# Kernel tuning notes

Hardware: AMD Instinct MI355X
Metric: run time of the kernel (lower is better)

Reference implementation:

```python
import jax, jax.numpy as jnp
import numpy as np

DILATIONS = (48, 76, 96, 111, 124, 135, 144, 152)


def setup_inputs() -> dict:
    key = jax.random.key(0)
    kx, kw, kb = jax.random.split(key, 3)
    B_, C_IN, H, Wd = 8, 64, 128, 512
    C_OUT = 64
    x = jax.random.normal(kx, (B_, C_IN, H, Wd), dtype=jnp.float32)
    # stacked weights for 8 parallel branches: [branch, out_ch, in_ch, kh=1, kw=3]
    W = jax.random.normal(kw, (8, C_OUT, C_IN, 1, 3), dtype=jnp.float32) * 0.05
    B = jax.random.normal(kb, (8, C_OUT), dtype=jnp.float32) * 0.05
    return {"x": x, "W": W, "B": B}


def _dilated_conv(x, w, d):
    # 'same' padding for kernel (1,3) with dilation (1,d): pad d on each side of width
    return jax.lax.conv_general_dilated(
        x, w,
        window_strides=(1, 1),
        padding=[(0, 0), (d, d)],
        rhs_dilation=(1, d),
        dimension_numbers=("NCHW", "OIHW", "NCHW"),
    )


def reference(x, W, B):
    out = None
    for i, d in enumerate(DILATIONS):  # fixed small structural loop over branches
        y = _dilated_conv(x, W[i], d) + B[i][None, :, None, None]
        out = y if out is None else out + y
    return jax.nn.relu(out)
```

## Files before the change

kernel.cpp:

```cpp
#include <hip/hip_runtime.h>
#include <hip/hip_bf16.h>
#include <stdint.h>

typedef float  f32x4 __attribute__((ext_vector_type(4)));
typedef short  s16x8 __attribute__((ext_vector_type(8)));

#define NB    8
#define CIN   64
#define COUT  64
#define HH    128
#define WW    512
#define NTAP  17
#define PADW  152
#define XROW  816
#define BUFB  (XROW * 64)
#define HW    (HH * WW)

__global__ __launch_bounds__(256) void prep_wfrag(
        const float* __restrict__ W, const float* __restrict__ Bv,
        __hip_bfloat16* __restrict__ wf, float* __restrict__ bsum) {
    int idx = blockIdx.x * 256 + threadIdx.x;
    if (idx < NTAP * 2 * 4 * 64 * 8) {
        int j  = idx & 7;
        int l  = (idx >> 3) & 63;
        int m  = (idx >> 9) & 3;
        int pp = (idx >> 11) & 1;
        int t  = idx >> 12;
        int ci = pp * 32 + 8 * (l >> 4) + j;
        int co = 16 * m + (l & 15);
        float v;
        if (t == 0) {
            v = 0.f;
            #pragma unroll
            for (int i = 0; i < NB; ++i) v += W[((i * COUT + co) * CIN + ci) * 3 + 1];
        } else if (t <= 8) {
            v = W[(((t - 1) * COUT + co) * CIN + ci) * 3 + 0];
        } else {
            v = W[(((t - 9) * COUT + co) * CIN + ci) * 3 + 2];
        }
        wf[idx] = __float2bfloat16(v);
    }
    if (idx < COUT) {
        float s = 0.f;
        #pragma unroll
        for (int i = 0; i < NB; ++i) s += Bv[i * COUT + idx];
        bsum[idx] = s;
    }
}

static constexpr int OFFS[NTAP] = {0, -48, -76, -96, -111, -124, -135, -144, -152,
                                      48,  76,  96,  111,  124,  135,  144,  152};

#define SB __builtin_amdgcn_sched_barrier(0)

#define LOADAF(AF, T0, CNT)                                                    \
    _Pragma("unroll")                                                          \
    for (int i = 0; i < (CNT); ++i)                                            \
        _Pragma("unroll")                                                      \
        for (int m = 0; m < 4; ++m)                                            \
            AF[i][m] = *reinterpret_cast<const s16x8*>(                        \
                wbase + ((T0) + i) * 8192 + m * 1024);

#define COMPTAPS(AF, T0, CNT)                                                  \
    _Pragma("unroll")                                                          \
    for (int i = 0; i < (CNT); ++i) {                                          \
        const int t      = (T0) + i;                                           \
        const int ldsrow = rowb + OFFS[t];                                     \
        const int slot   = lhi ^ ((ldsrow >> 1) & 3);                          \
        const char* bbase = smem + ldsrow * 64 + slot * 16;                    \
        s16x8 bfr[8];                                                          \
        _Pragma("unroll")                                                      \
        for (int n = 0; n < 8; ++n)                                            \
            bfr[n] = *reinterpret_cast<const s16x8*>(bbase + n * 1024);        \
        _Pragma("unroll")                                                      \
        for (int m = 0; m < 4; ++m)                                            \
            _Pragma("unroll")                                                  \
            for (int n = 0; n < 8; ++n)                                        \
                acc[m][n] = __builtin_amdgcn_mfma_f32_16x16x32_bf16(           \
                    AF[i][m], bfr[n], acc[m][n], 0, 0, 0);                     \
    }

__global__ __launch_bounds__(256, 2) void hdc_mfma(
        const float* __restrict__ x, const __hip_bfloat16* __restrict__ wf,
        const float* __restrict__ bsum, float* __restrict__ out) {
    __shared__ __align__(16) char smem[BUFB];

    const int tid  = threadIdx.x;
    const int wv   = tid >> 6;
    const int lane = tid & 63;
    const int l15  = lane & 15;
    const int lhi  = lane >> 4;
    const int c    = wv;
    const int wl   = tid & 63;
    const int row  = blockIdx.x;
    const int b    = row >> 7, h = row & 127;
    const int wlo  = wv * 128;
    const int rowb = PADW + wlo + l15;

    f32x4 acc[4][8];
    #pragma unroll
    for (int m = 0; m < 4; ++m) {
        f32x4 bi = *reinterpret_cast<const f32x4*>(bsum + 16 * m + 4 * lhi);
        #pragma unroll
        for (int n = 0; n < 8; ++n) acc[m][n] = bi;
    }

    {
        const int4 z{0, 0, 0, 0};
        int4* base = reinterpret_cast<int4*>(smem);
        for (int f = tid; f < 608; f += 256) {
            base[f] = z;
            base[2656 + f] = z;
        }
    }

    float4 xv[8];

    auto SLOAD = [&](int p, int hf) {
        const float* src = x +
            (((size_t)(b * CIN + p * 32 + c * 8) * HH + h) * WW) +
            hf * 256 + wl * 4;
        #pragma unroll
        for (int j = 0; j < 8; ++j)
            xv[j] = *reinterpret_cast<const float4*>(src + j * HW);
    };
    auto SWRITE = [&](int hf) {
        #pragma unroll
        for (int k = 0; k < 4; ++k) {
            const int r    = PADW + hf * 256 + wl * 4 + k;
            const int slot = c ^ ((r >> 1) & 3);
            union { __hip_bfloat16 hs[8]; int4 iv; } pk;
            #pragma unroll
            for (int j = 0; j < 8; ++j)
                pk.hs[j] = __float2bfloat16(((const float*)&xv[j])[k]);
            *reinterpret_cast<int4*>(smem + r * 64 + slot * 16) = pk.iv;
        }
    };

    SLOAD(0, 0); SWRITE(0);
    SLOAD(0, 1); SWRITE(1);
    __syncthreads();

    #pragma unroll
    for (int p = 0; p < 2; ++p) {
        const char* wbase = (const char*)wf + p * 4096 + lane * 16;

        s16x8 afA[2][4], afB[2][4];

        LOADAF(afA, 0, 2)    SB;
        LOADAF(afB, 2, 2)    SB;
        COMPTAPS(afA, 0, 2)  SB;
        LOADAF(afA, 4, 2)    SB;
        COMPTAPS(afB, 2, 2)  SB;
        LOADAF(afB, 6, 2)    SB;
        COMPTAPS(afA, 4, 2)  SB;
        LOADAF(afA, 8, 2)    SB;
        COMPTAPS(afB, 6, 2)  SB;
        LOADAF(afB, 10, 2)   SB;
        COMPTAPS(afA, 8, 2)  SB;
        LOADAF(afA, 12, 2)   SB;
        COMPTAPS(afB, 10, 2) SB;
        LOADAF(afB, 14, 2)   SB;
        COMPTAPS(afA, 12, 2) SB;
        LOADAF(afA, 16, 1)   SB;
        if (p == 0) SLOAD(1, 0);
        SB;
        COMPTAPS(afB, 14, 2) SB;
        COMPTAPS(afA, 16, 1) SB;

        __syncthreads();

        if (p == 0) {
            SWRITE(0);
            SLOAD(1, 1);
            SWRITE(1);
            __syncthreads();
        }
    }

    float* obase = out + (((size_t)b * COUT + 4 * lhi) * HH + h) * WW + wlo + l15;
    #pragma unroll
    for (int m = 0; m < 4; ++m)
        #pragma unroll
        for (int n = 0; n < 8; ++n)
            #pragma unroll
            for (int rr = 0; rr < 4; ++rr) {
                float v = acc[m][n][rr];
                obase[(size_t)(16 * m + rr) * HW + 16 * n] = v > 0.f ? v : 0.f;
            }
}

#define CI_STAGE 16

__global__ void prep_weff_fb(const float* __restrict__ W, const float* __restrict__ Bv,
                             float* __restrict__ weff, float* __restrict__ bsum) {
    int idx = blockIdx.x * 256 + threadIdx.x;
    if (idx < CIN * NTAP * COUT) {
        int co = idx & 63;
        int t  = (idx >> 6) % NTAP;
        int ci = idx / (NTAP * COUT);
        float v;
        if (t == 0) {
            v = 0.f;
            #pragma unroll
            for (int i = 0; i < NB; ++i) v += W[(((i * COUT + co) * CIN + ci) * 3) + 1];
        } else if (t <= 8) {
            v = W[((((t - 1) * COUT + co) * CIN + ci) * 3) + 0];
        } else {
            v = W[((((t - 9) * COUT + co) * CIN + ci) * 3) + 2];
        }
        weff[(ci * NTAP + t) * COUT + co] = v;
    }
    if (idx < COUT) {
        float s = 0.f;
        #pragma unroll
        for (int i = 0; i < NB; ++i) s += Bv[i * COUT + idx];
        bsum[idx] = s;
    }
}

__global__ __launch_bounds__(256, 2) void hdc_fb(
        const float* __restrict__ x, const float* __restrict__ weff,
        const float* __restrict__ bsum, float* __restrict__ out) {
    __shared__ float xsf[CI_STAGE][XROW];
    const int bh  = blockIdx.x;
    const int b   = bh >> 7;
    const int h   = bh & (HH - 1);
    const int tid = threadIdx.x;
    const int cg  = tid >> 5;
    const int wl  = tid & 31;
    float acc[8][16];
    #pragma unroll
    for (int j = 0; j < 8; ++j) {
        const float bj = bsum[cg * 8 + j];
        #pragma unroll
        for (int i = 0; i < 16; ++i) acc[j][i] = bj;
    }
    const float* xrowbase = x + ((size_t)(b * CIN) * HH + h) * WW;
    for (int s = 0; s < CIN / CI_STAGE; ++s) {
        __syncthreads();
        for (int f = tid; f < CI_STAGE * PADW; f += 256) {
            int r = f / PADW, cc = f - r * PADW;
            xsf[r][cc] = 0.f;
            xsf[r][PADW + WW + cc] = 0.f;
        }
        #pragma unroll
        for (int j = 0; j < 8; ++j) {
            int flat = j * 256 + tid;
            int r = flat >> 7, c4 = flat & 127;
            const float4 v = *reinterpret_cast<const float4*>(
                xrowbase + (size_t)(s * CI_STAGE + r) * HW + c4 * 4);
            *reinterpret_cast<float4*>(&xsf[r][PADW + c4 * 4]) = v;
        }
        __syncthreads();
        for (int r = 0; r < CI_STAGE; ++r) {
            const int ci = s * CI_STAGE + r;
            const float* wrow = weff + (size_t)(ci * NTAP) * COUT + cg * 8;
            const float* xr   = &xsf[r][PADW + wl];
            #pragma unroll
            for (int t = 0; t < NTAP; ++t) {
                const float4 w0 = *reinterpret_cast<const float4*>(wrow + t * COUT);
                const float4 w1 = *reinterpret_cast<const float4*>(wrow + t * COUT + 4);
                float xvv[16];
                #pragma unroll
                for (int i = 0; i < 16; ++i) xvv[i] = xr[OFFS[t] + 32 * i];
                const float wv2[8] = {w0.x, w0.y, w0.z, w0.w, w1.x, w1.y, w1.z, w1.w};
                #pragma unroll
                for (int j = 0; j < 8; ++j)
                    #pragma unroll
                    for (int i = 0; i < 16; ++i)
                        acc[j][i] = fmaf(wv2[j], xvv[i], acc[j][i]);
            }
        }
    }
    float* outbase = out + (((size_t)b * COUT + cg * 8) * HH + h) * WW + wl;
    #pragma unroll
    for (int j = 0; j < 8; ++j)
        #pragma unroll
        for (int i = 0; i < 16; ++i) {
            float v = acc[j][i];
            outbase[(size_t)j * HW + 32 * i] = v > 0.f ? v : 0.f;
        }
}


extern "C" void kernel_launch(void* const* d_in, const int* in_sizes, int n_in,
                              void* d_out, int out_size, void* d_ws, size_t ws_size,
                              hipStream_t stream) {
    const float* x  = (const float*)d_in[0];
    const float* W  = (const float*)d_in[1];
    const float* Bv = (const float*)d_in[2];
    float* out = (float*)d_out;

    const size_t need = 139264 + 256;

    if (ws_size >= need) {
        __hip_bfloat16* wf = (__hip_bfloat16*)d_ws;
        float* bsum = (float*)((char*)d_ws + 139264);
        prep_wfrag<<<272, 256, 0, stream>>>(W, Bv, wf, bsum);
        hdc_mfma<<<1024, 256, 0, stream>>>(x, wf, bsum, out);
    } else {
        float* weff = (float*)d_ws;
        float* bsum = weff + (size_t)CIN * NTAP * COUT;
        prep_weff_fb<<<(CIN * NTAP * COUT + 255) / 256, 256, 0, stream>>>(W, Bv, weff, bsum);
        hdc_fb<<<NB * HH, 256, 0, stream>>>(x, weff, bsum, out);
    }
}
```

Measured before the change: 88.26 us.

## Switch MFMA tiles from 16x16x32 to 32x32x16 bf16 with re-laid weight fragments

Replaces the 16x16x32 bf16 MFMA tiling with 32x32x16 tiles. Weight fragments are re-packed into 2 M-tiles by 2 K-chunks, the LDS B reads become two 8-element loads per 32-column tile, and the accumulator and output index mapping are reworked to match. The aim is fewer LDS loads per MFMA FLOP and fewer MFMA issues, since larger tiles reuse each operand fragment more. The tap loop is also restructured into a single-tap double-buffered schedule, which gives a different overlap of weight loads with compute.

```diff
diff --git a/kernel.cpp b/kernel.cpp
--- a/kernel.cpp
+++ b/kernel.cpp
@@ -2,8 +2,9 @@
 #include <hip/hip_bf16.h>
 #include <stdint.h>
 
-typedef float  f32x4 __attribute__((ext_vector_type(4)));
-typedef short  s16x8 __attribute__((ext_vector_type(8)));
+typedef float  f32x4  __attribute__((ext_vector_type(4)));
+typedef float  f32x16 __attribute__((ext_vector_type(16)));
+typedef short  s16x8  __attribute__((ext_vector_type(8)));
 
 #define NB    8
 #define CIN   64
@@ -20,14 +21,15 @@
         const float* __restrict__ W, const float* __restrict__ Bv,
         __hip_bfloat16* __restrict__ wf, float* __restrict__ bsum) {
     int idx = blockIdx.x * 256 + threadIdx.x;
-    if (idx < NTAP * 2 * 4 * 64 * 8) {
+    if (idx < NTAP * 2 * 2 * 2 * 64 * 8) {
         int j  = idx & 7;
         int l  = (idx >> 3) & 63;
-        int m  = (idx >> 9) & 3;
+        int kc = (idx >> 9) & 1;
+        int mt = (idx >> 10) & 1;
         int pp = (idx >> 11) & 1;
         int t  = idx >> 12;
-        int ci = pp * 32 + 8 * (l >> 4) + j;
-        int co = 16 * m + (l & 15);
+        int ci = pp * 32 + kc * 16 + 8 * (l >> 5) + j;
+        int co = mt * 32 + (l & 31);
         float v;
         if (t == 0) {
             v = 0.f;
@@ -53,31 +55,30 @@
 
 #define SB __builtin_amdgcn_sched_barrier(0)
 
-#define LOADAF(AF, T0, CNT)                                                    \
+#define LOADAF(AF, T)                                                          \
     _Pragma("unroll")                                                          \
-    for (int i = 0; i < (CNT); ++i)                                            \
+    for (int mt = 0; mt < 2; ++mt)                                             \
         _Pragma("unroll")                                                      \
-        for (int m = 0; m < 4; ++m)                                            \
-            AF[i][m] = *reinterpret_cast<const s16x8*>(                        \
-                wbase + ((T0) + i) * 8192 + m * 1024);
-
-#define COMPTAPS(AF, T0, CNT)                                                  \
+        for (int kc = 0; kc < 2; ++kc)                                         \
+            AF[mt][kc] = *reinterpret_cast<const s16x8*>(                      \
+                wbase + (T) * 8192 + (mt * 2 + kc) * 1024);
+
+#define COMPTAP(AF, T)                                                         \
     _Pragma("unroll")                                                          \
-    for (int i = 0; i < (CNT); ++i) {                                          \
-        const int t      = (T0) + i;                                           \
-        const int ldsrow = rowb + OFFS[t];                                     \
-        const int slot   = lhi ^ ((ldsrow >> 1) & 3);                          \
-        const char* bbase = smem + ldsrow * 64 + slot * 16;                    \
-        s16x8 bfr[8];                                                          \
-        _Pragma("unroll")                                                      \
-        for (int n = 0; n < 8; ++n)                                            \
-            bfr[n] = *reinterpret_cast<const s16x8*>(bbase + n * 1024);        \
-        _Pragma("unroll")                                                      \
-        for (int m = 0; m < 4; ++m)                                            \
-            _Pragma("unroll")                                                  \
-            for (int n = 0; n < 8; ++n)                                        \
-                acc[m][n] = __builtin_amdgcn_mfma_f32_16x16x32_bf16(           \
-                    AF[i][m], bfr[n], acc[m][n], 0, 0, 0);                     \
+    for (int nt = 0; nt < 4; ++nt) {                                           \
+        const int r_   = rowb + nt * 32 + OFFS[T];                             \
+        const int s0   = l5 ^ ((r_ >> 1) & 3);                                 \
+        const char* ba = smem + r_ * 64;                                       \
+        s16x8 bf0 = *reinterpret_cast<const s16x8*>(ba + s0 * 16);             \
+        s16x8 bf1 = *reinterpret_cast<const s16x8*>(ba + (s0 ^ 2) * 16);       \
+        acc[0][nt] = __builtin_amdgcn_mfma_f32_32x32x16_bf16(                  \
+            AF[0][0], bf0, acc[0][nt], 0, 0, 0);                               \
+        acc[0][nt] = __builtin_amdgcn_mfma_f32_32x32x16_bf16(                  \
+            AF[0][1], bf1, acc[0][nt], 0, 0, 0);                               \
+        acc[1][nt] = __builtin_amdgcn_mfma_f32_32x32x16_bf16(                  \
+            AF[1][0], bf0, acc[1][nt], 0, 0, 0);                               \
+        acc[1][nt] = __builtin_amdgcn_mfma_f32_32x32x16_bf16(                  \
+            AF[1][1], bf1, acc[1][nt], 0, 0, 0);                               \
     }
 
 __global__ __launch_bounds__(256, 2) void hdc_mfma(
@@ -88,22 +89,28 @@
     const int tid  = threadIdx.x;
     const int wv   = tid >> 6;
     const int lane = tid & 63;
-    const int l15  = lane & 15;
-    const int lhi  = lane >> 4;
+    const int l31  = lane & 31;
+    const int l5   = lane >> 5;
     const int c    = wv;
     const int wl   = tid & 63;
     const int row  = blockIdx.x;
     const int b    = row >> 7, h = row & 127;
     const int wlo  = wv * 128;
-    const int rowb = PADW + wlo + l15;
-
-    f32x4 acc[4][8];
-    #pragma unroll
-    for (int m = 0; m < 4; ++m) {
-        f32x4 bi = *reinterpret_cast<const f32x4*>(bsum + 16 * m + 4 * lhi);
-        #pragma unroll
-        for (int n = 0; n < 8; ++n) acc[m][n] = bi;
-    }
+    const int rowb = PADW + wlo + l31;
+
+    f32x16 acc[2][4];
+    #pragma unroll
+    for (int mt = 0; mt < 2; ++mt)
+        #pragma unroll
+        for (int rq = 0; rq < 4; ++rq) {
+            const f32x4 bi = *reinterpret_cast<const f32x4*>(
+                bsum + mt * 32 + 8 * rq + 4 * l5);
+            #pragma unroll
+            for (int nt = 0; nt < 4; ++nt)
+                #pragma unroll
+                for (int e = 0; e < 4; ++e)
+                    acc[mt][nt][4 * rq + e] = bi[e];
+        }
 
     {
         const int4 z{0, 0, 0, 0};
@@ -145,28 +152,17 @@
     for (int p = 0; p < 2; ++p) {
         const char* wbase = (const char*)wf + p * 4096 + lane * 16;
 
-        s16x8 afA[2][4], afB[2][4];
-
-        LOADAF(afA, 0, 2)    SB;
-        LOADAF(afB, 2, 2)    SB;
-        COMPTAPS(afA, 0, 2)  SB;
-        LOADAF(afA, 4, 2)    SB;
-        COMPTAPS(afB, 2, 2)  SB;
-        LOADAF(afB, 6, 2)    SB;
-        COMPTAPS(afA, 4, 2)  SB;
-        LOADAF(afA, 8, 2)    SB;
-        COMPTAPS(afB, 6, 2)  SB;
-        LOADAF(afB, 10, 2)   SB;
-        COMPTAPS(afA, 8, 2)  SB;
-        LOADAF(afA, 12, 2)   SB;
-        COMPTAPS(afB, 10, 2) SB;
-        LOADAF(afB, 14, 2)   SB;
-        COMPTAPS(afA, 12, 2) SB;
-        LOADAF(afA, 16, 1)   SB;
+        s16x8 afA[2][2], afB[2][2];
+
+        LOADAF(afA, 0) SB;
+        #pragma unroll
+        for (int t = 0; t < 16; ++t) {
+            if (t & 1) { LOADAF(afA, t + 1) SB; COMPTAP(afB, t) SB; }
+            else       { LOADAF(afB, t + 1) SB; COMPTAP(afA, t) SB; }
+        }
         if (p == 0) SLOAD(1, 0);
         SB;
-        COMPTAPS(afB, 14, 2) SB;
-        COMPTAPS(afA, 16, 1) SB;
+        COMPTAP(afA, 16) SB;
 
         __syncthreads();
 
@@ -178,15 +174,16 @@
         }
     }
 
-    float* obase = out + (((size_t)b * COUT + 4 * lhi) * HH + h) * WW + wlo + l15;
-    #pragma unroll
-    for (int m = 0; m < 4; ++m)
-        #pragma unroll
-        for (int n = 0; n < 8; ++n)
-            #pragma unroll
-            for (int rr = 0; rr < 4; ++rr) {
-                float v = acc[m][n][rr];
-                obase[(size_t)(16 * m + rr) * HW + 16 * n] = v > 0.f ? v : 0.f;
+    float* obase = out + (((size_t)b * COUT + 4 * l5) * HH + h) * WW + wlo + l31;
+    #pragma unroll
+    for (int mt = 0; mt < 2; ++mt)
+        #pragma unroll
+        for (int nt = 0; nt < 4; ++nt)
+            #pragma unroll
+            for (int r = 0; r < 16; ++r) {
+                const int co_off = mt * 32 + (r & 3) + 8 * (r >> 2);
+                float v = acc[mt][nt][r];
+                obase[(size_t)co_off * HW + nt * 32] = v > 0.f ? v : 0.f;
             }
 }
 
```

Measured after the change: 88.20 us. About the same (-0.1%).
